# Kernel tuning notes

Hardware: AMD Instinct MI355X
Metric: run time of the kernel (lower is better)

The kernel has to match this reference:

```python
import jax, jax.numpy as jnp
import numpy as np

P, E, N = 5, 400000, 50000  # edge types (protocols), edges per type, nodes
NEG_SLOPE = 0.2  # GATv2 leaky_relu default
LAYERS = ["e1", "e2", "e3", "d1", "d2", "d3"]  # encoder 15->8->8->2, decoder 2->8->8->15
DIMS = {"e1": (15, 8), "e2": (8, 8), "e3": (8, 2), "d1": (2, 8), "d2": (8, 8), "d3": (8, 15)}


def setup_inputs() -> dict:
    key = jax.random.key(0)
    ks = iter(jax.random.split(key, 64))

    def p(shape):
        return jax.random.normal(next(ks), shape, dtype=jnp.float32) * 0.1

    inp = {
        "x": jax.random.normal(next(ks), (N, 15), dtype=jnp.float32),
        "edge_attr": jax.random.normal(next(ks), (P, E, 35), dtype=jnp.float32),
        "edge_index": jax.random.randint(next(ks), (P, 2, E), 0, N, dtype=jnp.int32),
    }
    for name, (fi, fo) in DIMS.items():
        inp[f"{name}_wl"] = p((P, fi, fo))
        inp[f"{name}_wr"] = p((P, fi, fo))
        inp[f"{name}_we"] = p((P, 35, fo))
        inp[f"{name}_a"] = p((P, fo))
        inp[f"{name}_b"] = p((P, fo))
    return inp


def _hetero_gatv2(x, edge_index, edge_attr, Wl, Wr, We, att, b):
    """One to_hetero GATv2 layer: per-edge-type GATv2Conv (heads=1, add_self_loops=True,
    fill_value='mean' for self-loop edge_attr), summed over edge types."""
    n = x.shape[0]
    loop = jnp.arange(n, dtype=edge_index.dtype)

    def one(ei, ea, wl, wr, we, a, bb):
        xl = x @ wl  # [N, F] source-side projection
        xr = x @ wr  # [N, F] target-side projection
        s = jnp.concatenate([ei[0], loop])  # add self loops
        d = jnp.concatenate([ei[1], loop])
        # self-loop edge features = mean of edge_attr; project before concat to stay small
        eproj = jnp.concatenate(
            [ea @ we, jnp.broadcast_to(ea.mean(0) @ we, (n, wl.shape[1]))], axis=0
        )  # [E+N, F]
        m = xl[s] + xr[d] + eproj
        e = jax.nn.leaky_relu(m, NEG_SLOPE) @ a  # [E+N] attention logits
        emax = jax.ops.segment_max(e, d, num_segments=n)
        ex = jnp.exp(e - emax[d])
        den = jax.ops.segment_sum(ex, d, num_segments=n)
        alpha = ex / den[d]
        out = jax.ops.segment_sum(alpha[:, None] * xl[s], d, num_segments=n)
        return out + bb

    return jax.vmap(one)(edge_index, edge_attr, Wl, Wr, We, att, b).sum(0)


def _gae(x, edge_index, edge_attr, params):
    h = x
    for name in LAYERS:
        wl, wr, we, a, b = params[name]
        h = _hetero_gatv2(h, edge_index, edge_attr, wl, wr, we, a, b)
        if name not in ("e3", "d3"):  # relu between layers, none after enc/dec output
            h = jax.nn.relu(h)
    return h  # reconstruction [N, 15]


def reference(x, edge_attr, edge_index,
              e1_wl, e1_wr, e1_we, e1_a, e1_b,
              e2_wl, e2_wr, e2_we, e2_a, e2_b,
              e3_wl, e3_wr, e3_we, e3_a, e3_b,
              d1_wl, d1_wr, d1_we, d1_a, d1_b,
              d2_wl, d2_wr, d2_we, d2_a, d2_b,
              d3_wl, d3_wr, d3_we, d3_a, d3_b):
    params = {
        "e1": (e1_wl, e1_wr, e1_we, e1_a, e1_b),
        "e2": (e2_wl, e2_wr, e2_we, e2_a, e2_b),
        "e3": (e3_wl, e3_wr, e3_we, e3_a, e3_b),
        "d1": (d1_wl, d1_wr, d1_we, d1_a, d1_b),
        "d2": (d2_wl, d2_wr, d2_we, d2_a, d2_b),
        "d3": (d3_wl, d3_wr, d3_we, d3_a, d3_b),
    }
    return _gae(x, edge_index, edge_attr, params)
```

## Files before the change

### kernel.cpp

```cpp
#include <hip/hip_runtime.h>
#include <stdint.h>

#define PP 5
#define EE 400000
#define NN 50000
#define PN (PP*NN)
#define EPT (PP*EE)
#define G2 408
#define NGRP (EE/64)
#define NBK ((NN+255)/256)
#define NBKT (PP*NBK)
#define CHUNK 4096
#define NB2 ((EE+CHUNK-1)/CHUNK)

typedef unsigned int u32;
typedef unsigned short u16;
typedef unsigned char u8;
typedef float f32x4 __attribute__((ext_vector_type(4)));
typedef short s16x8 __attribute__((ext_vector_type(8)));
union FAB { s16x8 v; u32 w[4]; };

__device__ __forceinline__ u16 f2bf(float x){
  u32 u = __float_as_uint(x);
  u32 r = (u + 0x7fffu + ((u>>16)&1u))>>16;
  return (u16)r;
}
__device__ __forceinline__ u32 packbf(float a, float b){
  return (u32)f2bf(a) | ((u32)f2bf(b)<<16);
}
__device__ __forceinline__ float bf2f(u32 b){ return __uint_as_float(b<<16); }
__device__ __forceinline__ float lrelu(float x){ return fmaxf(x,0.f)+0.2f*fminf(x,0.f); }

__global__ __launch_bounds__(256) void k_bhist(const int* __restrict__ ei, u32* __restrict__ hist){
  __shared__ u32 sb[NBK];
  const int p=blockIdx.y, blk=blockIdx.x, t=threadIdx.x;
  for(int i=t;i<NBK;i+=256) sb[i]=0u;
  __syncthreads();
  const int* drow = ei + (size_t)(p*2+1)*EE;
  #pragma unroll
  for(int i=0;i<4;i++){
    int e = blk*CHUNK + i*1024 + t*4;
    if(e<EE){
      int4 d4=*(const int4*)&drow[e];
      atomicAdd(&sb[d4.x>>8],1u); atomicAdd(&sb[d4.y>>8],1u);
      atomicAdd(&sb[d4.z>>8],1u); atomicAdd(&sb[d4.w>>8],1u);
    }
  }
  __syncthreads();
  for(int i=t;i<NBK;i+=256) hist[((size_t)(p*NBK+i))*NB2 + blk]=sb[i];
}

__global__ __launch_bounds__(128) void k_bsum(u32* __restrict__ hist, u32* __restrict__ bcnt){
  __shared__ u32 s[128];
  const int g = blockIdx.y*NBK + blockIdx.x;
  const int t = threadIdx.x;
  u32 v = (t<NB2)? hist[(size_t)g*NB2+t] : 0u;
  s[t]=v; __syncthreads();
  for(int o=1;o<128;o<<=1){
    u32 x=(t>=o)?s[t-o]:0u;
    __syncthreads();
    s[t]+=x;
    __syncthreads();
  }
  if(t<NB2) hist[(size_t)g*NB2+t] = s[t]-v;
  if(t==127) bcnt[g]=s[127];
}

__global__ __launch_bounds__(1024) void k_bscan(const u32* __restrict__ bcnt, u32* __restrict__ boff){
  __shared__ u32 s[1024];
  const int t=threadIdx.x;
  u32 v=(t<NBKT)?bcnt[t]:0u;
  s[t]=v; __syncthreads();
  for(int o=1;o<1024;o<<=1){
    u32 x=(t>=o)?s[t-o]:0u;
    __syncthreads();
    s[t]+=x;
    __syncthreads();
  }
  if(t<NBKT) boff[t]=s[t]-v;
  if(t==0) boff[NBKT]=(u32)EPT;
}

__global__ __launch_bounds__(256) void k_bscatter2(const int* __restrict__ ei, const u32* __restrict__ boff,
                                                   const u32* __restrict__ hist, uint2* __restrict__ bedge){
  __shared__ u32 cur[NBK];
  const int p=blockIdx.y, blk=blockIdx.x, t=threadIdx.x;
  if(t<NBK) cur[t] = boff[p*NBK+t] + hist[((size_t)(p*NBK+t))*NB2 + blk];
  __syncthreads();
  const int* srow = ei + (size_t)(p*2  )*EE;
  const int* drow = ei + (size_t)(p*2+1)*EE;
  #pragma unroll
  for(int i=0;i<4;i++){
    int e = blk*CHUNK + i*1024 + t*4;
    if(e<EE){
      int4 s4=*(const int4*)&srow[e];
      int4 d4=*(const int4*)&drow[e];
      u32 p0=atomicAdd(&cur[d4.x>>8],1u);
      u32 p1=atomicAdd(&cur[d4.y>>8],1u);
      u32 p2=atomicAdd(&cur[d4.z>>8],1u);
      u32 p3=atomicAdd(&cur[d4.w>>8],1u);
      bedge[p0]=make_uint2((u32)s4.x|((u32)(d4.x&255)<<16),(u32)(e  ));
      bedge[p1]=make_uint2((u32)s4.y|((u32)(d4.y&255)<<16),(u32)(e+1));
      bedge[p2]=make_uint2((u32)s4.z|((u32)(d4.z&255)<<16),(u32)(e+2));
      bedge[p3]=make_uint2((u32)s4.w|((u32)(d4.w&255)<<16),(u32)(e+3));
    }
  }
}

__global__ __launch_bounds__(256) void k_bfinal2(const uint2* __restrict__ bedge, const u32* __restrict__ boff,
                                                 u32* __restrict__ off, u16* __restrict__ srcs16,
                                                 u32* __restrict__ eid){
  __shared__ u32 ncnt[256];
  __shared__ u32 lcur[256];
  const int p=blockIdx.y, b=blockIdx.x, t=threadIdx.x;
  const u32 g=(u32)(p*NBK+b);
  const u32 j0=boff[g], j1=boff[g+1], cnt=j1-j0;
  ncnt[t]=0u; __syncthreads();
  for(u32 i=t;i<cnt;i+=256){
    uint2 v=bedge[j0+i];
    atomicAdd(&ncnt[(v.x>>16)&255u],1u);
  }
  __syncthreads();
  u32 myc=ncnt[t];
  for(int o=1;o<256;o<<=1){
    u32 x=(t>=o)?ncnt[t-o]:0u;
    __syncthreads();
    ncnt[t]+=x;
    __syncthreads();
  }
  const u32 excl=ncnt[t]-myc;
  const int n0=b*256;
  if(n0+t<NN) off[(size_t)p*NN + n0 + t] = j0 + excl;
  if(g==NBKT-1 && t==0) off[PN]=(u32)EPT;
  lcur[t]=j0+excl;
  __syncthreads();
  for(u32 i=t;i<cnt;i+=256){
    uint2 v=bedge[j0+i];
    u32 dl=(v.x>>16)&255u;
    u32 pos=atomicAdd(&lcur[dl],1u);
    srcs16[pos]=(u16)(v.x&0xffffu);
    eid[pos]=v.y;
  }
}

__global__ __launch_bounds__(256) void k_eproj_mfma(
    const float* __restrict__ ea, const u32* __restrict__ eid,
    const float* __restrict__ we0, const float* __restrict__ we1,
    const float* __restrict__ we2, const float* __restrict__ we3,
    const float* __restrict__ we4, const float* __restrict__ we5,
    u16* __restrict__ ep0, u16* __restrict__ ep1, u16* __restrict__ ep2,
    u16* __restrict__ ep3, u16* __restrict__ ep4, u16* __restrict__ ep5,
    float* __restrict__ bpartP)
{
  __shared__ u16  sW[64*64];
  __shared__ u16  sEpi[4*16*72];
  __shared__ float sRed[64];

  const int t=threadIdx.x, p=blockIdx.y;
  const int w=t>>6, L=t&63, e16=L&15, quad=L>>4;

  for(int i=t;i<2048;i+=256) ((u32*)sW)[i]=0u;
  if(t<64) sRed[t]=0.f;
  __syncthreads();

  #define FILLW(WPTR,FO,MOFF) { const float* wsrc=(WPTR)+(size_t)p*35*(FO); \
    for(int i=t;i<35*(FO);i+=256){ int k=i/(FO), f=i-k*(FO); \
      sW[((MOFF)+f)*64+k]=f2bf(wsrc[i]); } }
  FILLW(we0,8,0) FILLW(we1,8,8) FILLW(we2,2,16) FILLW(we3,8,24) FILLW(we4,8,32) FILLW(we5,15,48)
  #undef FILLW
  __syncthreads();

  FAB afr[4][2];
  #pragma unroll
  for(int mt=0;mt<4;mt++)
    #pragma unroll
    for(int kf=0;kf<2;kf++)
      afr[mt][kf].v = *(const s16x8*)&sW[(e16+16*mt)*64 + kf*32 + quad*8];

  float sumacc[16];
  #pragma unroll
  for(int i=0;i<16;i++) sumacc[i]=0.f;

  u16* const myEpi = &sEpi[w*1152];

  u32 eedge_next = eid[(size_t)p*EE + (size_t)blockIdx.x*64 + w*16 + e16];

  for(int g=blockIdx.x; g<NGRP; g+=G2){
    const size_t jbase = (size_t)p*EE + (size_t)g*64 + w*16;

    const u32 eedge = eedge_next;
    {
      const int gn = g + G2;
      if(gn < NGRP)
        eedge_next = eid[(size_t)p*EE + (size_t)gn*64 + w*16 + e16];
    }

    const float* row = ea + ((size_t)p*EE + eedge)*35;
    float v0=row[quad*8+0], v1=row[quad*8+1], v2=row[quad*8+2], v3=row[quad*8+3];
    float v4=row[quad*8+4], v5=row[quad*8+5], v6=row[quad*8+6], v7=row[quad*8+7];
    float b0=0.f,b1=0.f,b2=0.f;
    if(quad==0){ b0=row[32]; b1=row[33]; b2=row[34]; }

    FAB fa, fb;
    fa.w[0]=packbf(v0,v1); fa.w[1]=packbf(v2,v3);
    fa.w[2]=packbf(v4,v5); fa.w[3]=packbf(v6,v7);
    fb.w[0]=packbf(b0,b1); fb.w[1]=packbf(b2,0.f);
    fb.w[2]=0u; fb.w[3]=0u;

    f32x4 acc0={0,0,0,0},acc1={0,0,0,0},acc2={0,0,0,0},acc3={0,0,0,0};
    acc0=__builtin_amdgcn_mfma_f32_16x16x32_bf16(afr[0][0].v, fa.v, acc0,0,0,0);
    acc0=__builtin_amdgcn_mfma_f32_16x16x32_bf16(afr[0][1].v, fb.v, acc0,0,0,0);
    acc1=__builtin_amdgcn_mfma_f32_16x16x32_bf16(afr[1][0].v, fa.v, acc1,0,0,0);
    acc1=__builtin_amdgcn_mfma_f32_16x16x32_bf16(afr[1][1].v, fb.v, acc1,0,0,0);
    acc2=__builtin_amdgcn_mfma_f32_16x16x32_bf16(afr[2][0].v, fa.v, acc2,0,0,0);
    acc2=__builtin_amdgcn_mfma_f32_16x16x32_bf16(afr[2][1].v, fb.v, acc2,0,0,0);
    acc3=__builtin_amdgcn_mfma_f32_16x16x32_bf16(afr[3][0].v, fa.v, acc3,0,0,0);
    acc3=__builtin_amdgcn_mfma_f32_16x16x32_bf16(afr[3][1].v, fb.v, acc3,0,0,0);

    #pragma unroll
    for(int r=0;r<4;r++){ sumacc[r]+=acc0[r]; sumacc[4+r]+=acc1[r]; sumacc[8+r]+=acc2[r]; sumacc[12+r]+=acc3[r]; }

    {
      u16* erow=&myEpi[e16*72];
      uint2 q;
      q.x=packbf(acc0[0],acc0[1]); q.y=packbf(acc0[2],acc0[3]);
      *(uint2*)(erow +  0 + 4*quad)=q;
      q.x=packbf(acc1[0],acc1[1]); q.y=packbf(acc1[2],acc1[3]);
      *(uint2*)(erow + 16 + 4*quad)=q;
      q.x=packbf(acc2[0],acc2[1]); q.y=packbf(acc2[2],acc2[3]);
      *(uint2*)(erow + 32 + 4*quad)=q;
      q.x=packbf(acc3[0],acc3[1]); q.y=packbf(acc3[2],acc3[3]);
      *(uint2*)(erow + 48 + 4*quad)=q;
    }
    asm volatile("s_waitcnt lgkmcnt(0)" ::: "memory");

    {
      const int grp=L>>4, e=L&15;
      const u16* erow=&myEpi[e*72];
      if(grp==0)      ((uint4*)ep0)[jbase+e]=*(const uint4*)(erow+ 0);
      else if(grp==1) ((uint4*)ep1)[jbase+e]=*(const uint4*)(erow+ 8);
      else if(grp==2) ((uint4*)ep3)[jbase+e]=*(const uint4*)(erow+24);
      else            ((uint4*)ep4)[jbase+e]=*(const uint4*)(erow+32);
      if(L<32){
        const int e2=L>>1, half=L&1;
        ((uint4*)ep5)[(jbase+e2)*2+half]=*(const uint4*)(&myEpi[e2*72]+48+8*half);
      } else if(L<48){
        const int e2=L-32;
        ((u32*)ep2)[jbase+e2]=*(const u32*)(&myEpi[e2*72]+16);
      }
    }
  }

  #pragma unroll
  for(int i=0;i<16;i++){
    float v=sumacc[i];
    v+=__shfl_xor(v,1); v+=__shfl_xor(v,2); v+=__shfl_xor(v,4); v+=__shfl_xor(v,8);
    sumacc[i]=v;
  }
  if(e16==0){
    #pragma unroll
    for(int mt=0;mt<4;mt++)
      #pragma unroll
      for(int r=0;r<4;r++)
        atomicAdd(&sRed[16*mt+4*quad+r], sumacc[mt*4+r]);
  }
  __syncthreads();
  if(t<64) bpartP[((size_t)p*G2+blockIdx.x)*64+t]=sRed[t];
}

__global__ __launch_bounds__(64) void k_selfvec3(const float* __restrict__ bpartP, float* __restrict__ selfvec){
  const int b=blockIdx.x;
  const int p=b>>6, m=b&63, t=threadIdx.x;
  float s=0.f;
  for(int i=t;i<G2;i+=64) s+=bpartP[((size_t)p*G2+i)*64+m];
  s+=__shfl_xor(s,1); s+=__shfl_xor(s,2); s+=__shfl_xor(s,4);
  s+=__shfl_xor(s,8); s+=__shfl_xor(s,16); s+=__shfl_xor(s,32);
  if(t==0){
    s*=(1.f/EE);
    int l=-1, f=0;
    if(m<8){l=0;f=m;} else if(m<16){l=1;f=m-8;} else if(m<18){l=2;f=m-16;}
    else if(m>=24&&m<32){l=3;f=m-24;} else if(m>=32&&m<40){l=4;f=m-32;}
    else if(m>=48&&m<63){l=5;f=m-48;}
    if(l>=0) selfvec[(size_t)(l*5+p)*16+f]=s;
  }
}

template<int FI,int FO>
__global__ __launch_bounds__(256) void k_proj(
  const float* __restrict__ h, int hs,
  const float* __restrict__ wl, const float* __restrict__ wr,
  float* __restrict__ xl, float* __restrict__ xr)
{
  __shared__ float sl[FI*FO], sr[FI*FO];
  const int t=threadIdx.x, p=blockIdx.y;
  if(t<FI*FO){ sl[t]=wl[(size_t)p*FI*FO+t]; sr[t]=wr[(size_t)p*FI*FO+t]; }
  __syncthreads();
  const int n=blockIdx.x*256+t;
  if(n>=NN) return;
  float hv[FI];
  #pragma unroll
  for(int k=0;k<FI;k++) hv[k]=h[(size_t)n*hs+k];
  const size_t base=((size_t)p*NN+n)*FO;
  #pragma unroll
  for(int f=0;f<FO;f++){
    float al=0.f, ar=0.f;
    #pragma unroll
    for(int k=0;k<FI;k++){ al+=hv[k]*sl[k*FO+f]; ar+=hv[k]*sr[k*FO+f]; }
    xl[base+f]=al; xr[base+f]=ar;
  }
}

template<int FI,int FO,int PO,bool RELU>
__global__ __launch_bounds__(256) void k_comb(
  const float* __restrict__ partial, const float* __restrict__ b,
  const float* __restrict__ wl, const float* __restrict__ wr,
  float* __restrict__ xl, float* __restrict__ xr)
{
  __shared__ float sl[5*FI*FO], sr[5*FI*FO], sbias[FI];
  const int t=threadIdx.x;
  for(int i=t;i<5*FI*FO;i+=256){ sl[i]=wl[i]; sr[i]=wr[i]; }
  if(t<FI){ float s=0.f; for(int p=0;p<PP;p++) s+=b[p*FI+t]; sbias[t]=s; }
  __syncthreads();
  const int n=blockIdx.x*256+t;
  if(n>=NN) return;
  float h[FI];
  #pragma unroll
  for(int f=0;f<FI;f++) h[f]=sbias[f];
  #pragma unroll
  for(int p=0;p<PP;p++){
    const float* src=partial+((size_t)p*NN+n)*FI;
    #pragma unroll
    for(int f=0;f<FI;f++) h[f]+=src[f];
  }
  if(RELU){
    #pragma unroll
    for(int f=0;f<FI;f++) h[f]=fmaxf(h[f],0.f);
  }
  #pragma unroll
  for(int p=0;p<PP;p++){
    const float* wlp=&sl[p*FI*FO];
    const float* wrp=&sr[p*FI*FO];
    const size_t base=((size_t)p*NN+n)*PO;
    #pragma unroll
    for(int f=0;f<FO;f++){
      float al=0.f, ar=0.f;
      #pragma unroll
      for(int k=0;k<FI;k++){ al+=h[k]*wlp[k*FO+f]; ar+=h[k]*wrp[k*FO+f]; }
      xl[base+f]=al; xr[base+f]=ar;
    }
    #pragma unroll
    for(int f=FO;f<PO;f++){ xl[base+f]=0.f; xr[base+f]=0.f; }
  }
}

template<int FO,int PO>
__device__ __forceinline__ void load_row(const float* __restrict__ g, float* arr){
  if constexpr(FO==2){
    float2 v=*(const float2*)g; arr[0]=v.x; arr[1]=v.y;
  } else {
    #pragma unroll
    for(int c=0;c<(FO+3)/4;c++){
      float4 v=((const float4*)g)[c];
      arr[4*c]=v.x;
      if(4*c+1<FO) arr[4*c+1]=v.y;
      if(4*c+2<FO) arr[4*c+2]=v.z;
      if(4*c+3<FO) arr[4*c+3]=v.w;
    }
  }
}

template<int FO,int EPAD,int PO>
__global__ __launch_bounds__(256) void k_agg(
  const float* __restrict__ xl, const float* __restrict__ xr,
  const u32* __restrict__ off, const u16* __restrict__ srcs16,
  const u16* __restrict__ ep, const float* __restrict__ avec,
  const float* __restrict__ selfv, float* __restrict__ partial)
{
  const int t=threadIdx.x, p=blockIdx.y;
  const int n=blockIdx.x*64+(t>>2), sub=t&3;
  if(n>=NN) return;
  const int r=p*NN+n;
  float av[FO], xln[FO], xrn[FO];
  #pragma unroll
  for(int f=0;f<FO;f++) av[f]=avec[p*FO+f];
  load_row<FO,PO>(xl+(size_t)r*PO, xln);
  load_row<FO,PO>(xr+(size_t)r*PO, xrn);

  float den=0.f, num[FO];
  #pragma unroll
  for(int f=0;f<FO;f++) num[f]=0.f;
  if(sub==0){
    float e=0.f;
    #pragma unroll
    for(int f=0;f<FO;f++){ float m=xln[f]+xrn[f]+selfv[p*16+f]; e+=lrelu(m)*av[f]; }
    float ex=__expf(e);
    den=ex;
    #pragma unroll
    for(int f=0;f<FO;f++) num[f]=ex*xln[f];
  }
  const u32 j1=off[r+1];
  for(u32 j=off[r]+sub;j<j1;j+=4){
    const u32 s=srcs16[j];
    float epv[FO];
    if constexpr(EPAD==8){
      uint4 q=*(const uint4*)(ep+(size_t)j*8);
      epv[0]=bf2f(q.x&0xffffu); epv[1]=bf2f(q.x>>16);
      epv[2]=bf2f(q.y&0xffffu); epv[3]=bf2f(q.y>>16);
      epv[4]=bf2f(q.z&0xffffu); epv[5]=bf2f(q.z>>16);
      epv[6]=bf2f(q.w&0xffffu); epv[7]=bf2f(q.w>>16);
    } else if constexpr(EPAD==2){
      u32 q=*(const u32*)(ep+(size_t)j*2);
      epv[0]=bf2f(q&0xffffu); epv[1]=bf2f(q>>16);
    } else {
      const uint4* qq=(const uint4*)(ep+(size_t)j*16);
      uint4 q0=qq[0], q1=qq[1];
      u32 w[8]={q0.x,q0.y,q0.z,q0.w,q1.x,q1.y,q1.z,q1.w};
      #pragma unroll
      for(int i=0;i<8;i++){
        if(2*i  <FO) epv[2*i  ]=bf2f(w[i]&0xffffu);
        if(2*i+1<FO) epv[2*i+1]=bf2f(w[i]>>16);
      }
    }
    float xls[FO];
    load_row<FO,PO>(xl+((size_t)p*NN+s)*PO, xls);
    float e=0.f;
    #pragma unroll
    for(int f=0;f<FO;f++){ float m=xls[f]+xrn[f]+epv[f]; e+=lrelu(m)*av[f]; }
    const float ex=__expf(e);
    den+=ex;
    #pragma unroll
    for(int f=0;f<FO;f++) num[f]+=ex*xls[f];
  }
  den+=__shfl_xor(den,1); den+=__shfl_xor(den,2);
  #pragma unroll
  for(int f=0;f<FO;f++){ num[f]+=__shfl_xor(num[f],1); num[f]+=__shfl_xor(num[f],2); }
  if(sub==0){
    const float inv=1.f/den;
    float* dst=partial+(size_t)r*PO;
    #pragma unroll
    for(int f=0;f<FO;f++) dst[f]=num[f]*inv;
  }
}

__global__ __launch_bounds__(256) void k_final15(
  const float* __restrict__ partial, const float* __restrict__ b,
  float* __restrict__ out)
{
  __shared__ float sbias[15];
  const int t=threadIdx.x;
  if(t<15){ float s=0.f; for(int p=0;p<PP;p++) s+=b[p*15+t]; sbias[t]=s; }
  __syncthreads();
  const int n=blockIdx.x*256+t;
  if(n>=NN) return;
  float s[15];
  #pragma unroll
  for(int f=0;f<15;f++) s[f]=sbias[f];
  #pragma unroll
  for(int p=0;p<PP;p++){
    const float* src=partial+((size_t)p*NN+n)*16;
    #pragma unroll
    for(int f=0;f<15;f++) s[f]+=src[f];
  }
  #pragma unroll
  for(int f=0;f<15;f++) out[(size_t)n*15+f]=s[f];
}

extern "C" void kernel_launch(void* const* d_in, const int* in_sizes, int n_in,
                              void* d_out, int out_size, void* d_ws, size_t ws_size,
                              hipStream_t stream)
{
  const float* x =(const float*)d_in[0];
  const float* ea=(const float*)d_in[1];
  const int*   ei=(const int*)d_in[2];
  auto W=[&](int l,int k)->const float*{ return (const float*)d_in[3+5*l+k]; };

  char* base=(char*)d_ws; size_t cur=0;
  auto alloc=[&](size_t bytes)->char*{ char* pp=base+cur; cur=(cur+bytes+255)&~(size_t)255; return pp; };
  u32*  off    =(u32*) alloc((size_t)(PN+1)*4);
  u32*  hist   =(u32*) alloc((size_t)NBKT*NB2*4);
  u32*  bcnt   =(u32*) alloc((size_t)NBKT*4);
  u32*  boff   =(u32*) alloc((size_t)(NBKT+1)*4);
  u16*  srcs16 =(u16*) alloc((size_t)EPT*2);
  u32*  eid    =(u32*) alloc((size_t)EPT*4);
  float* bpartP=(float*)alloc((size_t)PP*G2*64*4);
  float* selfvec=(float*)alloc(6*PP*16*4);
  float* xl    =(float*)alloc((size_t)PN*16*4);
  float* xr    =(float*)alloc((size_t)PN*16*4);
  float* partial=(float*)alloc((size_t)PN*16*4);
  u16*  ep0    =(u16*) alloc((size_t)EPT*8*2);
  u16*  ep1    =(u16*) alloc((size_t)EPT*8*2);
  u16*  ep2    =(u16*) alloc((size_t)EPT*2*2);
  u16*  ep3    =(u16*) alloc((size_t)EPT*8*2);
  u16*  ep4    =(u16*) alloc((size_t)EPT*8*2);
  u16*  ep5    =(u16*) alloc((size_t)EPT*16*2);
  uint2* bedge =(uint2*)ep5;
  (void)ws_size; (void)in_sizes; (void)n_in; (void)out_size;

  dim3 b256(256);
  k_bhist    <<<dim3(NB2,PP),b256,0,stream>>>(ei,hist);
  k_bsum     <<<dim3(NBK,PP),dim3(128),0,stream>>>(hist,bcnt);
  k_bscan    <<<dim3(1),dim3(1024),0,stream>>>(bcnt,boff);
  k_bscatter2<<<dim3(NB2,PP),b256,0,stream>>>(ei,boff,hist,bedge);
  k_bfinal2  <<<dim3(NBK,PP),b256,0,stream>>>(bedge,boff,off,srcs16,eid);
  k_eproj_mfma<<<dim3(G2,PP),b256,0,stream>>>(ea,eid,
              W(0,2),W(1,2),W(2,2),W(3,2),W(4,2),W(5,2),
              ep0,ep1,ep2,ep3,ep4,ep5,bpartP);
  k_selfvec3<<<dim3(PP*64),dim3(64),0,stream>>>(bpartP,selfvec);

  dim3 gproj((NN+255)/256,PP), gagg((NN+63)/64,PP), gnode((NN+255)/256);

  k_proj<15,8><<<gproj,b256,0,stream>>>(x,15,W(0,0),W(0,1),xl,xr);
  k_agg<8,8,8>   <<<gagg ,b256,0,stream>>>(xl,xr,off,srcs16,ep0,W(0,3),selfvec+0*80,partial);
  k_comb<8,8,8,true><<<gnode,b256,0,stream>>>(partial,W(0,4),W(1,0),W(1,1),xl,xr);
  k_agg<8,8,8>   <<<gagg ,b256,0,stream>>>(xl,xr,off,srcs16,ep1,W(1,3),selfvec+1*80,partial);
  k_comb<8,2,2,true><<<gnode,b256,0,stream>>>(partial,W(1,4),W(2,0),W(2,1),xl,xr);
  k_agg<2,2,2>   <<<gagg ,b256,0,stream>>>(xl,xr,off,srcs16,ep2,W(2,3),selfvec+2*80,partial);
  k_comb<2,8,8,false><<<gnode,b256,0,stream>>>(partial,W(2,4),W(3,0),W(3,1),xl,xr);
  k_agg<8,8,8>   <<<gagg ,b256,0,stream>>>(xl,xr,off,srcs16,ep3,W(3,3),selfvec+3*80,partial);
  k_comb<8,8,8,true><<<gnode,b256,0,stream>>>(partial,W(3,4),W(4,0),W(4,1),xl,xr);
  k_agg<8,8,8>   <<<gagg ,b256,0,stream>>>(xl,xr,off,srcs16,ep4,W(4,3),selfvec+4*80,partial);
  k_comb<8,15,16,true><<<gnode,b256,0,stream>>>(partial,W(4,4),W(5,0),W(5,1),xl,xr);
  k_agg<15,16,16><<<gagg ,b256,0,stream>>>(xl,xr,off,srcs16,ep5,W(5,3),selfvec+5*80,partial);
  k_final15<<<gnode,b256,0,stream>>>(partial,W(5,4),(float*)d_out);
}
```

Measured before the change: 803.8 us.

## Stage bucket edges in LDS and process two edges per thread in aggregation

```diff
diff --git a/kernel.cpp b/kernel.cpp
--- a/kernel.cpp
+++ b/kernel.cpp
@@ -12,6 +12,7 @@
 #define NBKT (PP*NBK)
 #define CHUNK 4096
 #define NB2 ((EE+CHUNK-1)/CHUNK)
+#define BCAP 3072
 
 typedef unsigned int u32;
 typedef unsigned short u16;
@@ -112,12 +113,15 @@
                                                  u32* __restrict__ eid){
   __shared__ u32 ncnt[256];
   __shared__ u32 lcur[256];
+  __shared__ uint2 sedge[BCAP];
   const int p=blockIdx.y, b=blockIdx.x, t=threadIdx.x;
   const u32 g=(u32)(p*NBK+b);
   const u32 j0=boff[g], j1=boff[g+1], cnt=j1-j0;
+  const bool fit=(cnt<=BCAP);
   ncnt[t]=0u; __syncthreads();
   for(u32 i=t;i<cnt;i+=256){
     uint2 v=bedge[j0+i];
+    if(fit) sedge[i]=v;
     atomicAdd(&ncnt[(v.x>>16)&255u],1u);
   }
   __syncthreads();
@@ -135,7 +139,7 @@
   lcur[t]=j0+excl;
   __syncthreads();
   for(u32 i=t;i<cnt;i+=256){
-    uint2 v=bedge[j0+i];
+    uint2 v = fit ? sedge[i] : bedge[j0+i];
     u32 dl=(v.x>>16)&255u;
     u32 pos=atomicAdd(&lcur[dl],1u);
     srcs16[pos]=(u16)(v.x&0xffffu);
@@ -369,6 +373,29 @@
   }
 }
 
+template<int FO,int EPAD>
+__device__ __forceinline__ void load_ep(const u16* __restrict__ ep, u32 j, float* epv){
+  if constexpr(EPAD==8){
+    uint4 q=*(const uint4*)(ep+(size_t)j*8);
+    epv[0]=bf2f(q.x&0xffffu); epv[1]=bf2f(q.x>>16);
+    epv[2]=bf2f(q.y&0xffffu); epv[3]=bf2f(q.y>>16);
+    epv[4]=bf2f(q.z&0xffffu); epv[5]=bf2f(q.z>>16);
+    epv[6]=bf2f(q.w&0xffffu); epv[7]=bf2f(q.w>>16);
+  } else if constexpr(EPAD==2){
+    u32 q=*(const u32*)(ep+(size_t)j*2);
+    epv[0]=bf2f(q&0xffffu); epv[1]=bf2f(q>>16);
+  } else {
+    const uint4* qq=(const uint4*)(ep+(size_t)j*16);
+    uint4 q0=qq[0], q1=qq[1];
+    u32 w[8]={q0.x,q0.y,q0.z,q0.w,q1.x,q1.y,q1.z,q1.w};
+    #pragma unroll
+    for(int i=0;i<8;i++){
+      if(2*i  <FO) epv[2*i  ]=bf2f(w[i]&0xffffu);
+      if(2*i+1<FO) epv[2*i+1]=bf2f(w[i]>>16);
+    }
+  }
+}
+
 template<int FO,int EPAD,int PO>
 __global__ __launch_bounds__(256) void k_agg(
   const float* __restrict__ xl, const float* __restrict__ xr,
@@ -380,16 +407,17 @@
   const int n=blockIdx.x*64+(t>>2), sub=t&3;
   if(n>=NN) return;
   const int r=p*NN+n;
-  float av[FO], xln[FO], xrn[FO];
+  float av[FO], xrn[FO];
   #pragma unroll
   for(int f=0;f<FO;f++) av[f]=avec[p*FO+f];
-  load_row<FO,PO>(xl+(size_t)r*PO, xln);
   load_row<FO,PO>(xr+(size_t)r*PO, xrn);
 
   float den=0.f, num[FO];
   #pragma unroll
   for(int f=0;f<FO;f++) num[f]=0.f;
   if(sub==0){
+    float xln[FO];
+    load_row<FO,PO>(xl+(size_t)r*PO, xln);
     float e=0.f;
     #pragma unroll
     for(int f=0;f<FO;f++){ float m=xln[f]+xrn[f]+selfv[p*16+f]; e+=lrelu(m)*av[f]; }
@@ -398,38 +426,29 @@
     #pragma unroll
     for(int f=0;f<FO;f++) num[f]=ex*xln[f];
   }
-  const u32 j1=off[r+1];
-  for(u32 j=off[r]+sub;j<j1;j+=4){
-    const u32 s=srcs16[j];
-    float epv[FO];
-    if constexpr(EPAD==8){
-      uint4 q=*(const uint4*)(ep+(size_t)j*8);
-      epv[0]=bf2f(q.x&0xffffu); epv[1]=bf2f(q.x>>16);
-      epv[2]=bf2f(q.y&0xffffu); epv[3]=bf2f(q.y>>16);
-      epv[4]=bf2f(q.z&0xffffu); epv[5]=bf2f(q.z>>16);
-      epv[6]=bf2f(q.w&0xffffu); epv[7]=bf2f(q.w>>16);
-    } else if constexpr(EPAD==2){
-      u32 q=*(const u32*)(ep+(size_t)j*2);
-      epv[0]=bf2f(q&0xffffu); epv[1]=bf2f(q>>16);
-    } else {
-      const uint4* qq=(const uint4*)(ep+(size_t)j*16);
-      uint4 q0=qq[0], q1=qq[1];
-      u32 w[8]={q0.x,q0.y,q0.z,q0.w,q1.x,q1.y,q1.z,q1.w};
-      #pragma unroll
-      for(int i=0;i<8;i++){
-        if(2*i  <FO) epv[2*i  ]=bf2f(w[i]&0xffffu);
-        if(2*i+1<FO) epv[2*i+1]=bf2f(w[i]>>16);
-      }
-    }
-    float xls[FO];
-    load_row<FO,PO>(xl+((size_t)p*NN+s)*PO, xls);
-    float e=0.f;
-    #pragma unroll
-    for(int f=0;f<FO;f++){ float m=xls[f]+xrn[f]+epv[f]; e+=lrelu(m)*av[f]; }
-    const float ex=__expf(e);
-    den+=ex;
-    #pragma unroll
-    for(int f=0;f<FO;f++) num[f]+=ex*xls[f];
+  const u32 j0=off[r], j1=off[r+1];
+  for(u32 j=j0+2*sub; j<j1; j+=8){
+    const bool hasB=(j+1<j1);
+    const u32 jB=hasB?(j+1):j;
+    const u32 sA=srcs16[j];
+    const u32 sB=srcs16[jB];
+    float epA[FO], epB[FO];
+    load_ep<FO,EPAD>(ep,j ,epA);
+    load_ep<FO,EPAD>(ep,jB,epB);
+    float xlsA[FO], xlsB[FO];
+    load_row<FO,PO>(xl+((size_t)p*NN+sA)*PO, xlsA);
+    load_row<FO,PO>(xl+((size_t)p*NN+sB)*PO, xlsB);
+    float eA=0.f, eB=0.f;
+    #pragma unroll
+    for(int f=0;f<FO;f++){
+      eA+=lrelu(xlsA[f]+xrn[f]+epA[f])*av[f];
+      eB+=lrelu(xlsB[f]+xrn[f]+epB[f])*av[f];
+    }
+    const float exA=__expf(eA);
+    const float exB=hasB?__expf(eB):0.f;
+    den+=exA+exB;
+    #pragma unroll
+    for(int f=0;f<FO;f++) num[f]+=exA*xlsA[f]+exB*xlsB[f];
   }
   den+=__shfl_xor(den,1); den+=__shfl_xor(den,2);
   #pragma unroll
```

Result: no change. 802.3 us (-0.2%).
